# Performance work log

Hardware: AMD Instinct MI355X
Metric: run time of the kernel (lower is better)

Reference implementation:

```python
import jax, jax.numpy as jnp
import numpy as np

N = 50000      # nodes
E = 800000     # edges (before self-loops)
F_IN = 128     # raw node feature dim
D = 500        # GCN_in_dim = gcn_dim = h_mlp_dim
T = 200000     # number of triplets


def setup_inputs() -> dict:
    key = jax.random.key(0)
    ks = jax.random.split(key, 13)
    s = 0.05
    return {
        "feats": jax.random.normal(ks[0], (N, F_IN), jnp.float32),
        "W_aff": jax.random.normal(ks[1], (F_IN, D), jnp.float32) * s,
        "b_aff": jax.random.normal(ks[2], (D,), jnp.float32) * s,
        "W_gcn": jax.random.normal(ks[3], (D, D), jnp.float32) * s,
        "b_gcn": jax.random.normal(ks[4], (D,), jnp.float32) * s,
        "W_pred_in": jax.random.normal(ks[5], (2 * D, D), jnp.float32) * s,
        "b_pred_in": jax.random.normal(ks[6], (D,), jnp.float32) * s,
        "W_pred_out": jax.random.normal(ks[7], (D, 1), jnp.float32) * s,
        "b_pred_out": jax.random.normal(ks[8], (1,), jnp.float32) * s,
        "src": jax.random.randint(ks[9], (E,), 0, N),
        "dst": jax.random.randint(ks[10], (E,), 0, N),
        "triplets": jax.random.randint(ks[11], (T, 3), 0, N),
    }


def reference(feats, W_aff, b_aff, W_gcn, b_gcn, W_pred_in, b_pred_in,
              W_pred_out, b_pred_out, src, dst, triplets):
    n = feats.shape[0]
    # LinearAffine (use_pre_linearAffine=True)
    x = feats @ W_aff + b_aff                      # [N, D]

    # dgl.add_self_loop
    loop = jnp.arange(n)
    s_idx = jnp.concatenate([src, loop])
    d_idx = jnp.concatenate([dst, loop])

    # GraphConv, norm='both', no edge weights, activation=None
    ones = jnp.ones(s_idx.shape[0], jnp.float32)
    out_deg = jax.ops.segment_sum(ones, s_idx, num_segments=n)
    in_deg = jax.ops.segment_sum(ones, d_idx, num_segments=n)
    norm_src = jnp.where(out_deg > 0, jax.lax.rsqrt(out_deg), 0.0)  # [N]
    norm_dst = jnp.where(in_deg > 0, jax.lax.rsqrt(in_deg), 0.0)    # [N]

    xw = x @ W_gcn                                  # [N, D]
    msg = xw[s_idx] * norm_src[s_idx, None]         # [E+N, D] gather
    agg = jax.ops.segment_sum(msg, d_idx, num_segments=n)  # scatter-add
    embedding = agg * norm_dst[:, None] + b_gcn     # [N, D]

    # triplet gather + MLP_edge_predictor (layer_num=2: cat->Linear->Linear)
    s_feat = embedding[triplets[:, 0]]              # [T, D]
    o_feat = embedding[triplets[:, 2]]              # [T, D]
    t = jnp.concatenate([s_feat, o_feat], axis=-1) @ W_pred_in + b_pred_in
    weights = t @ W_pred_out + b_pred_out           # [T, 1]
    return (weights, embedding)
```

## Files before the change

kernel.cpp:

```cpp
#include <hip/hip_runtime.h>


typedef float f32x4 __attribute__((ext_vector_type(4)));
typedef short s16x8 __attribute__((ext_vector_type(8)));

__device__ __forceinline__ unsigned short f2bf(float f) {
    unsigned u = __float_as_uint(f);
    unsigned r = (u + 0x7FFFu + ((u >> 16) & 1u)) >> 16;
    return (unsigned short)r;
}

__device__ __forceinline__ void async_ld16(const void* g, void* lds) {
    __builtin_amdgcn_global_load_lds(
        (const __attribute__((address_space(1))) unsigned int*)g,
        (__attribute__((address_space(3))) unsigned int*)lds,
        16, 0, 0);
}

__global__ __launch_bounds__(256) void hist2_kernel(
    const int* __restrict__ src, const int* __restrict__ dst,
    int* __restrict__ bhist_src, int* __restrict__ bhist_dst, int E) {
    __shared__ int lhs[256], lhd[256];
    lhs[threadIdx.x] = 0;
    lhd[threadIdx.x] = 0;
    __syncthreads();
    const int stride = gridDim.x * blockDim.x;
    for (int e = blockIdx.x * blockDim.x + threadIdx.x; e < E; e += stride) {
        atomicAdd(&lhs[src[e] >> 8], 1);
        atomicAdd(&lhd[dst[e] >> 8], 1);
    }
    __syncthreads();
    int cs = lhs[threadIdx.x], cd = lhd[threadIdx.x];
    if (cs > 0) atomicAdd(&bhist_src[threadIdx.x], cs);
    if (cd > 0) atomicAdd(&bhist_dst[threadIdx.x], cd);
}

__global__ void bscan2_kernel(const int* __restrict__ bhist_src, const int* __restrict__ bhist_dst,
                              int* __restrict__ sbbase, int* __restrict__ sbcursor,
                              int* __restrict__ dbbase, int* __restrict__ dbcursor,
                              int nbuk, int E) {
    __shared__ int sv[256];
    const int tid = threadIdx.x;

    int c = (tid < nbuk) ? bhist_src[tid] : 0;
    sv[tid] = c;
    __syncthreads();
    for (int st = 1; st < 256; st <<= 1) {
        int t = (tid >= st) ? sv[tid - st] : 0;
        __syncthreads();
        sv[tid] += t;
        __syncthreads();
    }
    if (tid < nbuk) { int ex = sv[tid] - c; sbbase[tid] = ex; sbcursor[tid] = ex; }
    if (tid == 0) sbbase[nbuk] = E;
    __syncthreads();

    c = (tid < nbuk) ? bhist_dst[tid] : 0;
    sv[tid] = c;
    __syncthreads();
    for (int st = 1; st < 256; st <<= 1) {
        int t = (tid >= st) ? sv[tid - st] : 0;
        __syncthreads();
        sv[tid] += t;
        __syncthreads();
    }
    if (tid < nbuk) { int ex = sv[tid] - c; dbbase[tid] = ex; dbcursor[tid] = ex; }
    if (tid == 0) dbbase[nbuk] = E;
}

#define PCH 4096
__global__ __launch_bounds__(256) void fused_partition_kernel(
    const int* __restrict__ src, const int* __restrict__ dst,
    int* __restrict__ dcursor, unsigned long long* __restrict__ pairs,
    int* __restrict__ scursor, int* __restrict__ ssorted,
    int E, int nbuk) {
    __shared__ int lhist[256];
    __shared__ int lbase[256];
    __shared__ int gbase[256];
    __shared__ int scanv[256];
    __shared__ unsigned long long lpair[PCH];
    __shared__ unsigned char lbid[PCH];

    const int tid = threadIdx.x;
    const int c0 = blockIdx.x * PCH;
    int cnt = E - c0; if (cnt > PCH) cnt = PCH;

    int dv[16], sv[16], rk[16];

    lhist[tid] = 0;
    __syncthreads();
#pragma unroll
    for (int q = 0; q < 16; ++q) {
        int e = c0 + q * 256 + tid;
        if (e < E) {
            int d = dst[e];
            dv[q] = d;
            sv[q] = src[e];
            rk[q] = atomicAdd(&lhist[d >> 8], 1);
        } else {
            dv[q] = -1;
            sv[q] = -1;
        }
    }
    __syncthreads();

    int c = lhist[tid];
    scanv[tid] = c;
    __syncthreads();
    for (int st = 1; st < 256; st <<= 1) {
        int t = (tid >= st) ? scanv[tid - st] : 0;
        __syncthreads();
        scanv[tid] += t;
        __syncthreads();
    }
    lbase[tid] = scanv[tid] - c;
    if (tid < nbuk && c > 0) gbase[tid] = atomicAdd(&dcursor[tid], c);
    __syncthreads();

#pragma unroll
    for (int q = 0; q < 16; ++q) {
        if (dv[q] >= 0) {
            int b = dv[q] >> 8;
            int slot = lbase[b] + rk[q];
            lpair[slot] = ((unsigned long long)(unsigned)dv[q] << 32) | (unsigned)sv[q];
            lbid[slot] = (unsigned char)b;
        }
    }
    __syncthreads();

    for (int i = tid; i < cnt; i += 256) {
        int b = lbid[i];
        pairs[(long)gbase[b] + (i - lbase[b])] = lpair[i];
    }
    __syncthreads();

    int* lval = (int*)lpair;
    lhist[tid] = 0;
    __syncthreads();
#pragma unroll
    for (int q = 0; q < 16; ++q) {
        if (sv[q] >= 0) rk[q] = atomicAdd(&lhist[sv[q] >> 8], 1);
    }
    __syncthreads();

    c = lhist[tid];
    scanv[tid] = c;
    __syncthreads();
    for (int st = 1; st < 256; st <<= 1) {
        int t = (tid >= st) ? scanv[tid - st] : 0;
        __syncthreads();
        scanv[tid] += t;
        __syncthreads();
    }
    lbase[tid] = scanv[tid] - c;
    if (tid < nbuk && c > 0) gbase[tid] = atomicAdd(&scursor[tid], c);
    __syncthreads();

#pragma unroll
    for (int q = 0; q < 16; ++q) {
        if (sv[q] >= 0) {
            int b = sv[q] >> 8;
            int slot = lbase[b] + rk[q];
            lval[slot] = sv[q];
            lbid[slot] = (unsigned char)b;
        }
    }
    __syncthreads();

    for (int i = tid; i < cnt; i += 256) {
        int b = lbid[i];
        ssorted[(long)gbase[b] + (i - lbase[b])] = lval[i];
    }
}

__global__ __launch_bounds__(256) void bucket_finalize_kernel(
    const unsigned long long* __restrict__ pairs, const int* __restrict__ dbbase,
    const int* __restrict__ ssorted, const int* __restrict__ sbbase,
    int* __restrict__ row_ptr, float* __restrict__ ndv,
    int* __restrict__ csr_src, float* __restrict__ ns, int N) {
    __shared__ int hist[256];
    __shared__ int scanv[256];
    __shared__ int lcur[256];
    const int tid = threadIdx.x;
    const int b = blockIdx.x;
    const int node = b * 256 + tid;

    const int e0 = dbbase[b], e1 = dbbase[b + 1];
    hist[tid] = 0;
    __syncthreads();
    for (int e = e0 + tid; e < e1; e += 256) {
        int d = (int)(pairs[e] >> 32);
        atomicAdd(&hist[d & 255], 1);
    }
    __syncthreads();

    int c = hist[tid];
    scanv[tid] = c;
    __syncthreads();
    for (int st = 1; st < 256; st <<= 1) {
        int t = (tid >= st) ? scanv[tid - st] : 0;
        __syncthreads();
        scanv[tid] += t;
        __syncthreads();
    }
    int excl = scanv[tid] - c;
    if (node < N) {
        row_ptr[node] = e0 + excl;
        ndv[node] = rsqrtf((float)(c + 1));
    }
    if (node == N) row_ptr[N] = e0 + excl;
    lcur[tid] = excl;
    __syncthreads();

    for (int e = e0 + tid; e < e1; e += 256) {
        unsigned long long pr = pairs[e];
        int d = (int)(pr >> 32);
        int r = atomicAdd(&lcur[d & 255], 1);
        csr_src[e0 + r] = (int)(pr & 0xFFFFFFFFu);
    }

    __syncthreads();
    hist[tid] = 0;
    __syncthreads();
    const int s0 = sbbase[b], s1 = sbbase[b + 1];
    for (int e = s0 + tid; e < s1; e += 256) atomicAdd(&hist[ssorted[e] & 255], 1);
    __syncthreads();
    if (node < N) ns[node] = rsqrtf((float)(hist[tid] + 1));
}

__global__ __launch_bounds__(256) void bcomb_part_kernel(
    const float* __restrict__ b_aff, const float* __restrict__ W_gcn,
    float* __restrict__ part, int D, int PD) {
    int n = blockIdx.x * blockDim.x + threadIdx.x;
    int c = blockIdx.y;
    if (n >= PD) return;
    float s = 0.f;
    if (n < D) {
        int k0 = c * 8;
        int k1 = k0 + 8; if (k1 > D) k1 = D;
        for (int k = k0; k < k1; ++k) s = fmaf(b_aff[k], W_gcn[(long)k * D + n], s);
    }
    part[(long)c * PD + n] = s;
}

__global__ void vcomb_kernel(const float* __restrict__ Win, const float* __restrict__ wout,
                             float* __restrict__ v, int D, int K2) {
    int k = blockIdx.x * (blockDim.x >> 6) + (threadIdx.x >> 6);
    int lane = threadIdx.x & 63;
    if (k >= K2) return;
    float s = 0.f;
    for (int c = lane; c < D; c += 64) s = fmaf(Win[(long)k * D + c], wout[c], s);
#pragma unroll
    for (int m = 32; m > 0; m >>= 1) s += __shfl_down(s, m);
    if (lane == 0) v[k] = s;
}

__global__ void bias_dot_kernel(const float* __restrict__ b_in, const float* __restrict__ w_out,
                                const float* __restrict__ b_out, float* __restrict__ bias_dot, int D) {
    __shared__ float sm[256];
    float s = 0.f;
    for (int c = threadIdx.x; c < D; c += 256) s = fmaf(b_in[c], w_out[c], s);
    sm[threadIdx.x] = s;
    __syncthreads();
    for (int st = 128; st > 0; st >>= 1) {
        if (threadIdx.x < st) sm[threadIdx.x] += sm[threadIdx.x + st];
        __syncthreads();
    }
    if (threadIdx.x == 0) bias_dot[0] = sm[0] + b_out[0];
}

__global__ void pad_kernel(const float* __restrict__ part, const float* __restrict__ b_gcn,
                           const float* __restrict__ v, float* __restrict__ bcp,
                           float* __restrict__ bgp, float* __restrict__ v1p,
                           float* __restrict__ v2p, int D, int PD, int NC) {
    int i = blockIdx.x * blockDim.x + threadIdx.x;
    if (i < PD) {
        float s = 0.f;
        for (int c = 0; c < NC; ++c) s += part[(long)c * PD + i];
        bcp[i] = s;
        bgp[i] = (i < D) ? b_gcn[i] : 0.f;
        v1p[i] = (i < D) ? v[i] : 0.f;
        v2p[i] = (i < D) ? v[D + i] : 0.f;
    }
}

__global__ __launch_bounds__(256) void sgemm_kernel(const float* __restrict__ A, int lda,
                                                    const float* __restrict__ B, int ldb,
                                                    float* __restrict__ C, int ldc,
                                                    int M, int N, int K) {
    __shared__ __align__(16) float As[16][68];
    __shared__ __align__(16) float Bs[16][68];
    const int tid = threadIdx.x;
    const int tx = tid & 15, ty = tid >> 4;
    const int row0 = blockIdx.x * 64;
    const int col0 = blockIdx.y * 64;

    const int a_row = tid >> 2;
    const int a_k   = (tid & 3) * 4;
    const int b_k   = tid >> 4;
    const int b_c   = (tid & 15) * 4;

    float acc[4][4] = {};

    for (int k0 = 0; k0 < K; k0 += 16) {
        float4 av = make_float4(0.f, 0.f, 0.f, 0.f);
        {
            int gr = row0 + a_row;
            int gk = k0 + a_k;
            if (gr < M) {
                if (gk + 3 < K) {
                    av = *reinterpret_cast<const float4*>(&A[(long)gr * lda + gk]);
                } else {
                    float t0 = (gk + 0 < K) ? A[(long)gr * lda + gk + 0] : 0.f;
                    float t1 = (gk + 1 < K) ? A[(long)gr * lda + gk + 1] : 0.f;
                    float t2 = (gk + 2 < K) ? A[(long)gr * lda + gk + 2] : 0.f;
                    float t3 = (gk + 3 < K) ? A[(long)gr * lda + gk + 3] : 0.f;
                    av = make_float4(t0, t1, t2, t3);
                }
            }
        }
        float4 bv = make_float4(0.f, 0.f, 0.f, 0.f);
        {
            int gk = k0 + b_k;
            int gc = col0 + b_c;
            if (gk < K) {
                if (gc + 3 < N) {
                    bv = *reinterpret_cast<const float4*>(&B[(long)gk * ldb + gc]);
                } else {
                    float t0 = (gc + 0 < N) ? B[(long)gk * ldb + gc + 0] : 0.f;
                    float t1 = (gc + 1 < N) ? B[(long)gk * ldb + gc + 1] : 0.f;
                    float t2 = (gc + 2 < N) ? B[(long)gk * ldb + gc + 2] : 0.f;
                    float t3 = (gc + 3 < N) ? B[(long)gk * ldb + gc + 3] : 0.f;
                    bv = make_float4(t0, t1, t2, t3);
                }
            }
        }
        __syncthreads();
        As[a_k + 0][a_row] = av.x;
        As[a_k + 1][a_row] = av.y;
        As[a_k + 2][a_row] = av.z;
        As[a_k + 3][a_row] = av.w;
        *reinterpret_cast<float4*>(&Bs[b_k][b_c]) = bv;
        __syncthreads();

#pragma unroll
        for (int k = 0; k < 16; ++k) {
            const float4 a = *reinterpret_cast<const float4*>(&As[k][ty * 4]);
            const float4 b = *reinterpret_cast<const float4*>(&Bs[k][tx * 4]);
            const float avv[4] = {a.x, a.y, a.z, a.w};
            const float bvv[4] = {b.x, b.y, b.z, b.w};
#pragma unroll
            for (int i = 0; i < 4; ++i)
#pragma unroll
                for (int j = 0; j < 4; ++j)
                    acc[i][j] = fmaf(avv[i], bvv[j], acc[i][j]);
        }
    }

#pragma unroll
    for (int i = 0; i < 4; ++i) {
        int r = row0 + ty * 4 + i;
        if (r >= M) continue;
#pragma unroll
        for (int j = 0; j < 4; ++j) {
            int c = col0 + tx * 4 + j;
            if (c < N) C[(long)r * ldc + c] = acc[i][j];
        }
    }
}

__global__ void conv_feats_kernel(const float* __restrict__ feats, const float* __restrict__ ns,
                                  unsigned short* __restrict__ fs16, int N) {
    int idx = blockIdx.x * blockDim.x + threadIdx.x;
    if (idx >= N * 16) return;
    int node = idx >> 4;
    int c = (idx & 15) * 8;
    float s = ns[node];
    const float* p = feats + (long)node * 128 + c;
    float4 a = *reinterpret_cast<const float4*>(p);
    float4 b = *reinterpret_cast<const float4*>(p + 4);
    uint4 o;
    o.x = (unsigned)f2bf(a.x * s) | ((unsigned)f2bf(a.y * s) << 16);
    o.y = (unsigned)f2bf(a.z * s) | ((unsigned)f2bf(a.w * s) << 16);
    o.z = (unsigned)f2bf(b.x * s) | ((unsigned)f2bf(b.y * s) << 16);
    o.w = (unsigned)f2bf(b.z * s) | ((unsigned)f2bf(b.w * s) << 16);
    *reinterpret_cast<uint4*>(fs16 + (long)node * 128 + c) = o;
}

__global__ void conv_Bt_kernel(const float* __restrict__ Wc, unsigned short* __restrict__ Bt,
                               int D, int PD) {
    int idx = blockIdx.x * blockDim.x + threadIdx.x;
    if (idx >= PD * 16) return;
    int n = idx >> 4;
    int k8 = (idx & 15) * 8;
    uint4 o = make_uint4(0, 0, 0, 0);
    if (n < D) {
        unsigned short t[8];
#pragma unroll
        for (int q = 0; q < 8; ++q) t[q] = f2bf(Wc[(long)(k8 + q) * D + n]);
        o.x = (unsigned)t[0] | ((unsigned)t[1] << 16);
        o.y = (unsigned)t[2] | ((unsigned)t[3] << 16);
        o.z = (unsigned)t[4] | ((unsigned)t[5] << 16);
        o.w = (unsigned)t[6] | ((unsigned)t[7] << 16);
    }
    *reinterpret_cast<uint4*>(Bt + (long)n * 128 + k8) = o;
}

__global__ __launch_bounds__(256) void gather_feats_kernel(
    const unsigned short* __restrict__ fs16, const int* __restrict__ csr_src,
    const int* __restrict__ row_ptr, const float* __restrict__ ns,
    unsigned short* __restrict__ g16, float* __restrict__ h, int N) {
    int d = blockIdx.x * 4 + (threadIdx.x >> 6);
    int lane = threadIdx.x & 63;
    if (d >= N) return;
    const int g = lane >> 4;
    const int fl = lane & 15;

    float a[8] = {0.f, 0.f, 0.f, 0.f, 0.f, 0.f, 0.f, 0.f};
    float hacc = 0.f;

    const int beg = row_ptr[d], end = row_ptr[d + 1];
    for (int j0 = beg; j0 < end; j0 += 64) {
        int cnt = end - j0;
        if (cnt > 64) cnt = 64;
        int s = (lane < cnt) ? csr_src[j0 + lane] : 0;
        if (lane < cnt) hacc += ns[s];
        for (int k = 0; k < cnt; k += 8) {
            int k0 = k + g, k1 = k + 4 + g;
            int i0 = __shfl(s, k0 & 63);
            int i1 = __shfl(s, k1 & 63);
            uint4 v0 = make_uint4(0u, 0u, 0u, 0u), v1 = make_uint4(0u, 0u, 0u, 0u);
            if (k0 < cnt) v0 = *reinterpret_cast<const uint4*>(fs16 + (long)i0 * 128 + fl * 8);
            if (k1 < cnt) v1 = *reinterpret_cast<const uint4*>(fs16 + (long)i1 * 128 + fl * 8);
            a[0] += __uint_as_float(v0.x << 16); a[1] += __uint_as_float(v0.x & 0xFFFF0000u);
            a[2] += __uint_as_float(v0.y << 16); a[3] += __uint_as_float(v0.y & 0xFFFF0000u);
            a[4] += __uint_as_float(v0.z << 16); a[5] += __uint_as_float(v0.z & 0xFFFF0000u);
            a[6] += __uint_as_float(v0.w << 16); a[7] += __uint_as_float(v0.w & 0xFFFF0000u);
            a[0] += __uint_as_float(v1.x << 16); a[1] += __uint_as_float(v1.x & 0xFFFF0000u);
            a[2] += __uint_as_float(v1.y << 16); a[3] += __uint_as_float(v1.y & 0xFFFF0000u);
            a[4] += __uint_as_float(v1.z << 16); a[5] += __uint_as_float(v1.z & 0xFFFF0000u);
            a[6] += __uint_as_float(v1.w << 16); a[7] += __uint_as_float(v1.w & 0xFFFF0000u);
        }
    }

#pragma unroll
    for (int r = 0; r < 8; ++r) {
        a[r] += __shfl_xor(a[r], 16);
        a[r] += __shfl_xor(a[r], 32);
    }
    {
        uint4 sv4 = *reinterpret_cast<const uint4*>(fs16 + (long)d * 128 + fl * 8);
        a[0] += __uint_as_float(sv4.x << 16); a[1] += __uint_as_float(sv4.x & 0xFFFF0000u);
        a[2] += __uint_as_float(sv4.y << 16); a[3] += __uint_as_float(sv4.y & 0xFFFF0000u);
        a[4] += __uint_as_float(sv4.z << 16); a[5] += __uint_as_float(sv4.z & 0xFFFF0000u);
        a[6] += __uint_as_float(sv4.w << 16); a[7] += __uint_as_float(sv4.w & 0xFFFF0000u);
    }
#pragma unroll
    for (int m = 32; m > 0; m >>= 1) hacc += __shfl_xor(hacc, m);
    if (lane == 0) h[d] = hacc + ns[d];
    if (lane < 16) {
        uint4 o;
        o.x = (unsigned)f2bf(a[0]) | ((unsigned)f2bf(a[1]) << 16);
        o.y = (unsigned)f2bf(a[2]) | ((unsigned)f2bf(a[3]) << 16);
        o.z = (unsigned)f2bf(a[4]) | ((unsigned)f2bf(a[5]) << 16);
        o.w = (unsigned)f2bf(a[6]) | ((unsigned)f2bf(a[7]) << 16);
        *reinterpret_cast<uint4*>(g16 + (long)d * 128 + fl * 8) = o;
    }
}

__global__ __launch_bounds__(256) void gcn_gemm_kernel(
    const unsigned short* __restrict__ g16, const unsigned short* __restrict__ Bt,
    const float* __restrict__ h, const float* __restrict__ nd,
    const float* __restrict__ bcp, const float* __restrict__ bgp,
    const float* __restrict__ v1p, const float* __restrict__ v2p,
    float* __restrict__ emb, float* __restrict__ u1, float* __restrict__ u2,
    int M, int D) {

    __shared__ __align__(16) unsigned short As[128 * 32];
    __shared__ __align__(16) unsigned short Bs[128 * 32];

    const int tid  = threadIdx.x;
    const int w    = tid >> 6;
    const int lane = tid & 63;
    const int row0 = blockIdx.x * 128;
    const int col0 = blockIdx.y * 128;

    const int r0   = 2 * w * 16 + (lane >> 2);
    const int r1   = (2 * w + 1) * 16 + (lane >> 2);
    const int slot = lane & 3;
    const int c0   = slot ^ ((r0 >> 1) & 3);
    const int c1   = slot ^ ((r1 >> 1) & 3);

    const unsigned short* pA0 = g16 + (long)(row0 + r0) * 128 + c0 * 8;
    const unsigned short* pA1 = g16 + (long)(row0 + r1) * 128 + c1 * 8;
    const unsigned short* pB0 = Bt + (long)(col0 + r0) * 128 + c0 * 8;
    const unsigned short* pB1 = Bt + (long)(col0 + r1) * 128 + c1 * 8;

    unsigned short* dA0 = As + 2 * w * 512;
    unsigned short* dA1 = As + (2 * w + 1) * 512;
    unsigned short* dB0 = Bs + 2 * w * 512;
    unsigned short* dB1 = Bs + (2 * w + 1) * 512;

    const int wrow = (w & 1) * 64;
    const int wcol = (w >> 1) * 64;
    const int lm = lane & 15, q = lane >> 4;
    const s16x8* pa[4];
    const s16x8* pb[4];
#pragma unroll
    for (int i = 0; i < 4; ++i) {
        int r = wrow + i * 16 + lm;
        int cs = q ^ ((r >> 1) & 3);
        pa[i] = reinterpret_cast<const s16x8*>(As + r * 32 + cs * 8);
        int n = wcol + i * 16 + lm;
        int cs2 = q ^ ((n >> 1) & 3);
        pb[i] = reinterpret_cast<const s16x8*>(Bs + n * 32 + cs2 * 8);
    }

    f32x4 acc[4][4];
#pragma unroll
    for (int i = 0; i < 4; ++i)
#pragma unroll
        for (int j = 0; j < 4; ++j) acc[i][j] = (f32x4)0.f;

    for (int k0 = 0; k0 < 128; k0 += 32) {
        async_ld16(pA0 + k0, dA0);
        async_ld16(pA1 + k0, dA1);
        async_ld16(pB0 + k0, dB0);
        async_ld16(pB1 + k0, dB1);
        __syncthreads();

        s16x8 af[4], bf[4];
#pragma unroll
        for (int i = 0; i < 4; ++i) { af[i] = *pa[i]; bf[i] = *pb[i]; }
#pragma unroll
        for (int i = 0; i < 4; ++i)
#pragma unroll
            for (int j = 0; j < 4; ++j)
                acc[i][j] = __builtin_amdgcn_mfma_f32_16x16x32_bf16(af[i], bf[j], acc[i][j], 0, 0, 0);
        __syncthreads();
    }

    float bcv[4], bgv[4], w1[4], w2[4];
    int colv[4];
#pragma unroll
    for (int j = 0; j < 4; ++j) {
        int c = col0 + wcol + j * 16 + lm;
        colv[j] = c;
        bcv[j] = bcp[c];
        bgv[j] = bgp[c];
        w1[j] = v1p[c];
        w2[j] = v2p[c];
    }

#pragma unroll
    for (int i = 0; i < 4; ++i) {
        float p1[4], p2[4];
#pragma unroll
        for (int reg = 0; reg < 4; ++reg) {
            int row = row0 + wrow + i * 16 + q * 4 + reg;
            float hb = h[row];
            float sc = nd[row];
            float s1 = 0.f, s2 = 0.f;
#pragma unroll
            for (int j = 0; j < 4; ++j) {
                float o = fmaf(sc, acc[i][j][reg] + hb * bcv[j], bgv[j]);
                if (row < M && colv[j] < D) emb[(long)row * D + colv[j]] = o;
                s1 = fmaf(o, w1[j], s1);
                s2 = fmaf(o, w2[j], s2);
            }
            p1[reg] = s1;
            p2[reg] = s2;
        }
#pragma unroll
        for (int mask = 1; mask < 16; mask <<= 1)
#pragma unroll
            for (int reg = 0; reg < 4; ++reg) {
                p1[reg] += __shfl_xor(p1[reg], mask);
                p2[reg] += __shfl_xor(p2[reg], mask);
            }
        if (lm == 0) {
#pragma unroll
            for (int reg = 0; reg < 4; ++reg) {
                int row = row0 + wrow + i * 16 + q * 4 + reg;
                if (row < M) {
                    atomicAdd(&u1[row], p1[reg]);
                    atomicAdd(&u2[row], p2[reg]);
                }
            }
        }
    }
}

__global__ void weights_kernel(const int* __restrict__ trip, const float* __restrict__ u1,
                               const float* __restrict__ u2, const float* __restrict__ bdot,
                               float* __restrict__ w, int T) {
    int r = blockIdx.x * blockDim.x + threadIdx.x;
    if (r < T) {
        int s = trip[(long)r * 3 + 0];
        int o = trip[(long)r * 3 + 2];
        w[r] = u1[s] + u2[o] + bdot[0];
    }
}


extern "C" void kernel_launch(void* const* d_in, const int* in_sizes, int n_in,
                              void* d_out, int out_size, void* d_ws, size_t ws_size,
                              hipStream_t stream) {
    const float* feats      = (const float*)d_in[0];
    const float* W_aff      = (const float*)d_in[1];
    const float* b_aff      = (const float*)d_in[2];
    const float* W_gcn      = (const float*)d_in[3];
    const float* b_gcn      = (const float*)d_in[4];
    const float* W_pred_in  = (const float*)d_in[5];
    const float* b_pred_in  = (const float*)d_in[6];
    const float* W_pred_out = (const float*)d_in[7];
    const float* b_pred_out = (const float*)d_in[8];
    const int*   src        = (const int*)d_in[9];
    const int*   dst        = (const int*)d_in[10];
    const int*   trip       = (const int*)d_in[11];

    const int D = in_sizes[2];
    const int F = in_sizes[1] / D;
    const int N = in_sizes[0] / F;
    const int E = in_sizes[9];
    const int T = in_sizes[11] / 3;

    const int PD = 512;
    const int GX = (N + 127) / 128;
    const int Mpad = GX * 128;
    const int NC = (D + 7) / 8;
    const int NBUK = (N >> 8) + 1;

    float* weights = (float*)d_out;
    float* emb     = (float*)d_out + T;

    char* p = (char*)d_ws;
    unsigned short* fs16 = (unsigned short*)p;  p += (size_t)N * 128 * 2;
    unsigned short* g16  = (unsigned short*)p;  p += (size_t)Mpad * 128 * 2;
    unsigned long long* pairs = (unsigned long long*)p; p += (size_t)E * 8;
    int* ssorted = (int*)p;  p += (size_t)E * 4;
    unsigned short* Bt   = (unsigned short*)p;  p += (size_t)PD * 128 * 2;
    float* Wc   = (float*)p;  p += (size_t)F * D * 4;
    float* bparts = (float*)p;  p += (size_t)64 * PD * 4;
    float* bcp  = (float*)p;  p += PD * 4;
    float* bgp  = (float*)p;  p += PD * 4;
    float* v1p  = (float*)p;  p += PD * 4;
    float* v2p  = (float*)p;  p += PD * 4;
    float* v    = (float*)p;  p += 1024 * 4;
    float* bdot = (float*)p;  p += 16;
    float* ns   = (float*)p;  p += (size_t)N * 4;
    float* nd   = (float*)p;  p += (size_t)N * 4;
    float* h    = (float*)p;  p += (size_t)Mpad * 4;
    float* u1   = (float*)p;  p += (size_t)N * 4;
    float* u2   = (float*)p;  p += (size_t)N * 4;
    int* bhist_src = (int*)p;  p += 256 * 4;
    int* bhist_dst = (int*)p;  p += 256 * 4;
    int* sbbase   = (int*)p;  p += 260 * 4;
    int* sbcursor = (int*)p;  p += 256 * 4;
    int* dbbase   = (int*)p;  p += 260 * 4;
    int* dbcursor = (int*)p;  p += 256 * 4;
    int* row_ptr = (int*)p;  p += (size_t)(N + 1) * 4;
    int* csr_src = (int*)p;  p += (size_t)E * 4;

    hipMemsetAsync(bhist_src, 0, 512 * 4, stream);
    hipMemsetAsync(u1, 0, 2 * (size_t)N * sizeof(float), stream);
    hipMemsetAsync(g16 + (size_t)N * 128, 0, (size_t)(Mpad - N) * 128 * 2, stream);
    hipMemsetAsync(h + N, 0, (size_t)(Mpad - N) * 4, stream);

    hist2_kernel<<<256, 256, 0, stream>>>(src, dst, bhist_src, bhist_dst, E);
    bscan2_kernel<<<1, 256, 0, stream>>>(bhist_src, bhist_dst, sbbase, sbcursor,
                                         dbbase, dbcursor, NBUK, E);
    fused_partition_kernel<<<(E + PCH - 1) / PCH, 256, 0, stream>>>(
        src, dst, dbcursor, pairs, sbcursor, ssorted, E, NBUK);
    bucket_finalize_kernel<<<NBUK, 256, 0, stream>>>(pairs, dbbase, ssorted, sbbase,
                                                     row_ptr, nd, csr_src, ns, N);

    vcomb_kernel<<<(2 * D + 3) / 4, 256, 0, stream>>>(W_pred_in, W_pred_out, v, D, 2 * D);
    bias_dot_kernel<<<1, 256, 0, stream>>>(b_pred_in, W_pred_out, b_pred_out, bdot, D);

    {
        dim3 grid((F + 63) / 64, (D + 63) / 64);
        sgemm_kernel<<<grid, 256, 0, stream>>>(W_aff, D, W_gcn, D, Wc, D, F, D, D);
    }
    {
        dim3 grid((PD + 255) / 256, NC);
        bcomb_part_kernel<<<grid, 256, 0, stream>>>(b_aff, W_gcn, bparts, D, PD);
    }
    pad_kernel<<<(PD + 255) / 256, 256, 0, stream>>>(bparts, b_gcn, v, bcp, bgp, v1p, v2p, D, PD, NC);
    conv_Bt_kernel<<<(PD * 16 + 255) / 256, 256, 0, stream>>>(Wc, Bt, D, PD);

    conv_feats_kernel<<<(N * 16 + 255) / 256, 256, 0, stream>>>(feats, ns, fs16, N);

    gather_feats_kernel<<<(N + 3) / 4, 256, 0, stream>>>(fs16, csr_src, row_ptr, ns, g16, h, N);

    {
        dim3 grid(GX, PD / 128);
        gcn_gemm_kernel<<<grid, 256, 0, stream>>>(g16, Bt, h, nd, bcp, bgp, v1p, v2p,
                                                  emb, u1, u2, N, D);
    }

    weights_kernel<<<(T + 255) / 256, 256, 0, stream>>>(trip, u1, u2, bdot, weights, T);
}
```

Measured before the change: 354.9 us.

## Fuse small setup kernels, split-K the weight-combine GEMM, fold feature conversion

Four memsets become one init kernel. The three small prep kernels (bias combine, predictor vector, bias dot) are merged into one launch. The Bt conversion now runs together with the pad kernel, and the bf16 feature conversion is folded into bucket_finalize. The small W_aff@W_gcn SGEMM is split along K into 4 partial products that the conversion kernel sums, which raises parallelism for a tiny-grid GEMM. This cuts launch count and serial latency, at the cost of a larger workspace and extra partial-sum reads.

Result: faster. 315.2 us (-11.2%).

```diff
diff --git a/kernel.cpp b/kernel.cpp
--- a/kernel.cpp
+++ b/kernel.cpp
@@ -15,6 +15,18 @@
         (const __attribute__((address_space(1))) unsigned int*)g,
         (__attribute__((address_space(3))) unsigned int*)lds,
         16, 0, 0);
+}
+
+__global__ __launch_bounds__(256) void init_kernel(
+    float* __restrict__ u, int nU4, unsigned* __restrict__ gpad, int nG,
+    float* __restrict__ hpad, int nH, int* __restrict__ bh, int nB) {
+    const int stride = gridDim.x * blockDim.x;
+    const int i0 = blockIdx.x * blockDim.x + threadIdx.x;
+    for (int i = i0; i < nU4; i += stride)
+        *reinterpret_cast<float4*>(u + i * 4) = make_float4(0.f, 0.f, 0.f, 0.f);
+    for (int i = i0; i < nG; i += stride) gpad[i] = 0u;
+    for (int i = i0; i < nH; i += stride) hpad[i] = 0.f;
+    for (int i = i0; i < nB; i += stride) bh[i] = 0;
 }
 
 __global__ __launch_bounds__(256) void hist2_kernel(
@@ -176,11 +188,14 @@
 __global__ __launch_bounds__(256) void bucket_finalize_kernel(
     const unsigned long long* __restrict__ pairs, const int* __restrict__ dbbase,
     const int* __restrict__ ssorted, const int* __restrict__ sbbase,
+    const float* __restrict__ feats,
     int* __restrict__ row_ptr, float* __restrict__ ndv,
-    int* __restrict__ csr_src, float* __restrict__ ns, int N) {
+    int* __restrict__ csr_src, float* __restrict__ ns,
+    unsigned short* __restrict__ fs16, int N) {
     __shared__ int hist[256];
     __shared__ int scanv[256];
     __shared__ int lcur[256];
+    __shared__ float nsv[256];
     const int tid = threadIdx.x;
     const int b = blockIdx.x;
     const int node = b * 256 + tid;
@@ -225,68 +240,78 @@
     const int s0 = sbbase[b], s1 = sbbase[b + 1];
     for (int e = s0 + tid; e < s1; e += 256) atomicAdd(&hist[ssorted[e] & 255], 1);
     __syncthreads();
-    if (node < N) ns[node] = rsqrtf((float)(hist[tid] + 1));
-}
-
-__global__ __launch_bounds__(256) void bcomb_part_kernel(
+    float nsval = rsqrtf((float)(hist[tid] + 1));
+    nsv[tid] = nsval;
+    if (node < N) ns[node] = nsval;
+    __syncthreads();
+
+    for (int r0 = 0; r0 < 256; r0 += 16) {
+        int r = r0 + (tid >> 4);
+        int nn = b * 256 + r;
+        if (nn >= N) break;
+        int cq = (tid & 15) * 8;
+        float s = nsv[r];
+        const float* pf = feats + (long)nn * 128 + cq;
+        float4 a = *reinterpret_cast<const float4*>(pf);
+        float4 d2 = *reinterpret_cast<const float4*>(pf + 4);
+        uint4 o;
+        o.x = (unsigned)f2bf(a.x * s) | ((unsigned)f2bf(a.y * s) << 16);
+        o.y = (unsigned)f2bf(a.z * s) | ((unsigned)f2bf(a.w * s) << 16);
+        o.z = (unsigned)f2bf(d2.x * s) | ((unsigned)f2bf(d2.y * s) << 16);
+        o.w = (unsigned)f2bf(d2.z * s) | ((unsigned)f2bf(d2.w * s) << 16);
+        *reinterpret_cast<uint4*>(fs16 + (long)nn * 128 + cq) = o;
+    }
+}
+
+__global__ __launch_bounds__(256) void prep1_kernel(
     const float* __restrict__ b_aff, const float* __restrict__ W_gcn,
-    float* __restrict__ part, int D, int PD) {
-    int n = blockIdx.x * blockDim.x + threadIdx.x;
-    int c = blockIdx.y;
-    if (n >= PD) return;
-    float s = 0.f;
-    if (n < D) {
-        int k0 = c * 8;
-        int k1 = k0 + 8; if (k1 > D) k1 = D;
-        for (int k = k0; k < k1; ++k) s = fmaf(b_aff[k], W_gcn[(long)k * D + n], s);
-    }
-    part[(long)c * PD + n] = s;
-}
-
-__global__ void vcomb_kernel(const float* __restrict__ Win, const float* __restrict__ wout,
-                             float* __restrict__ v, int D, int K2) {
-    int k = blockIdx.x * (blockDim.x >> 6) + (threadIdx.x >> 6);
-    int lane = threadIdx.x & 63;
-    if (k >= K2) return;
-    float s = 0.f;
-    for (int c = lane; c < D; c += 64) s = fmaf(Win[(long)k * D + c], wout[c], s);
-#pragma unroll
-    for (int m = 32; m > 0; m >>= 1) s += __shfl_down(s, m);
-    if (lane == 0) v[k] = s;
-}
-
-__global__ void bias_dot_kernel(const float* __restrict__ b_in, const float* __restrict__ w_out,
-                                const float* __restrict__ b_out, float* __restrict__ bias_dot, int D) {
+    float* __restrict__ part,
+    const float* __restrict__ Win, const float* __restrict__ wout,
+    float* __restrict__ v,
+    const float* __restrict__ b_in, const float* __restrict__ b_out,
+    float* __restrict__ bdot,
+    int D, int PD, int NBbc, int NBv, int nbper) {
     __shared__ float sm[256];
-    float s = 0.f;
-    for (int c = threadIdx.x; c < D; c += 256) s = fmaf(b_in[c], w_out[c], s);
-    sm[threadIdx.x] = s;
-    __syncthreads();
-    for (int st = 128; st > 0; st >>= 1) {
-        if (threadIdx.x < st) sm[threadIdx.x] += sm[threadIdx.x + st];
-        __syncthreads();
-    }
-    if (threadIdx.x == 0) bias_dot[0] = sm[0] + b_out[0];
-}
-
-__global__ void pad_kernel(const float* __restrict__ part, const float* __restrict__ b_gcn,
-                           const float* __restrict__ v, float* __restrict__ bcp,
-                           float* __restrict__ bgp, float* __restrict__ v1p,
-                           float* __restrict__ v2p, int D, int PD, int NC) {
-    int i = blockIdx.x * blockDim.x + threadIdx.x;
-    if (i < PD) {
+    const int b = blockIdx.x;
+    const int tid = threadIdx.x;
+
+    if (b < NBbc) {
+        int nblk = b % nbper;
+        int cch = b / nbper;
+        int n = nblk * 256 + tid;
+        if (n >= PD) return;
         float s = 0.f;
-        for (int c = 0; c < NC; ++c) s += part[(long)c * PD + i];
-        bcp[i] = s;
-        bgp[i] = (i < D) ? b_gcn[i] : 0.f;
-        v1p[i] = (i < D) ? v[i] : 0.f;
-        v2p[i] = (i < D) ? v[D + i] : 0.f;
+        if (n < D) {
+            int k0 = cch * 8;
+            int k1 = k0 + 8; if (k1 > D) k1 = D;
+            for (int k = k0; k < k1; ++k) s = fmaf(b_aff[k], W_gcn[(long)k * D + n], s);
+        }
+        part[(long)cch * PD + n] = s;
+    } else if (b < NBbc + NBv) {
+        int k = (b - NBbc) * 4 + (tid >> 6);
+        int lane = tid & 63;
+        if (k >= 2 * D) return;
+        float s = 0.f;
+        for (int cc = lane; cc < D; cc += 64) s = fmaf(Win[(long)k * D + cc], wout[cc], s);
+#pragma unroll
+        for (int m = 32; m > 0; m >>= 1) s += __shfl_down(s, m);
+        if (lane == 0) v[k] = s;
+    } else {
+        float s = 0.f;
+        for (int cc = tid; cc < D; cc += 256) s = fmaf(b_in[cc], wout[cc], s);
+        sm[tid] = s;
+        __syncthreads();
+        for (int st = 128; st > 0; st >>= 1) {
+            if (tid < st) sm[tid] += sm[tid + st];
+            __syncthreads();
+        }
+        if (tid == 0) bdot[0] = sm[0] + b_out[0];
     }
 }
 
 __global__ __launch_bounds__(256) void sgemm_kernel(const float* __restrict__ A, int lda,
                                                     const float* __restrict__ B, int ldb,
-                                                    float* __restrict__ C, int ldc,
+                                                    float* __restrict__ Cp, int ldc,
                                                     int M, int N, int K) {
     __shared__ __align__(16) float As[16][68];
     __shared__ __align__(16) float Bs[16][68];
@@ -294,6 +319,9 @@
     const int tx = tid & 15, ty = tid >> 4;
     const int row0 = blockIdx.x * 64;
     const int col0 = blockIdx.y * 64;
+    const int kbeg = blockIdx.z * 128;
+    int kend = kbeg + 128; if (kend > K) kend = K;
+    float* C = Cp + (long)blockIdx.z * M * ldc;
 
     const int a_row = tid >> 2;
     const int a_k   = (tid & 3) * 4;
@@ -302,19 +330,19 @@
 
     float acc[4][4] = {};
 
-    for (int k0 = 0; k0 < K; k0 += 16) {
+    for (int k0 = kbeg; k0 < kend; k0 += 16) {
         float4 av = make_float4(0.f, 0.f, 0.f, 0.f);
         {
             int gr = row0 + a_row;
             int gk = k0 + a_k;
             if (gr < M) {
-                if (gk + 3 < K) {
+                if (gk + 3 < kend) {
                     av = *reinterpret_cast<const float4*>(&A[(long)gr * lda + gk]);
                 } else {
-                    float t0 = (gk + 0 < K) ? A[(long)gr * lda + gk + 0] : 0.f;
-                    float t1 = (gk + 1 < K) ? A[(long)gr * lda + gk + 1] : 0.f;
-                    float t2 = (gk + 2 < K) ? A[(long)gr * lda + gk + 2] : 0.f;
-                    float t3 = (gk + 3 < K) ? A[(long)gr * lda + gk + 3] : 0.f;
+                    float t0 = (gk + 0 < kend) ? A[(long)gr * lda + gk + 0] : 0.f;
+                    float t1 = (gk + 1 < kend) ? A[(long)gr * lda + gk + 1] : 0.f;
+                    float t2 = (gk + 2 < kend) ? A[(long)gr * lda + gk + 2] : 0.f;
+                    float t3 = (gk + 3 < kend) ? A[(long)gr * lda + gk + 3] : 0.f;
                     av = make_float4(t0, t1, t2, t3);
                 }
             }
@@ -323,7 +351,7 @@
         {
             int gk = k0 + b_k;
             int gc = col0 + b_c;
-            if (gk < K) {
+            if (gk < kend) {
                 if (gc + 3 < N) {
                     bv = *reinterpret_cast<const float4*>(&B[(long)gk * ldb + gc]);
                 } else {
@@ -369,41 +397,46 @@
     }
 }
 
-__global__ void conv_feats_kernel(const float* __restrict__ feats, const float* __restrict__ ns,
-                                  unsigned short* __restrict__ fs16, int N) {
-    int idx = blockIdx.x * blockDim.x + threadIdx.x;
-    if (idx >= N * 16) return;
-    int node = idx >> 4;
-    int c = (idx & 15) * 8;
-    float s = ns[node];
-    const float* p = feats + (long)node * 128 + c;
-    float4 a = *reinterpret_cast<const float4*>(p);
-    float4 b = *reinterpret_cast<const float4*>(p + 4);
-    uint4 o;
-    o.x = (unsigned)f2bf(a.x * s) | ((unsigned)f2bf(a.y * s) << 16);
-    o.y = (unsigned)f2bf(a.z * s) | ((unsigned)f2bf(a.w * s) << 16);
-    o.z = (unsigned)f2bf(b.x * s) | ((unsigned)f2bf(b.y * s) << 16);
-    o.w = (unsigned)f2bf(b.z * s) | ((unsigned)f2bf(b.w * s) << 16);
-    *reinterpret_cast<uint4*>(fs16 + (long)node * 128 + c) = o;
-}
-
-__global__ void conv_Bt_kernel(const float* __restrict__ Wc, unsigned short* __restrict__ Bt,
-                               int D, int PD) {
-    int idx = blockIdx.x * blockDim.x + threadIdx.x;
-    if (idx >= PD * 16) return;
-    int n = idx >> 4;
-    int k8 = (idx & 15) * 8;
-    uint4 o = make_uint4(0, 0, 0, 0);
-    if (n < D) {
-        unsigned short t[8];
-#pragma unroll
-        for (int q = 0; q < 8; ++q) t[q] = f2bf(Wc[(long)(k8 + q) * D + n]);
-        o.x = (unsigned)t[0] | ((unsigned)t[1] << 16);
-        o.y = (unsigned)t[2] | ((unsigned)t[3] << 16);
-        o.z = (unsigned)t[4] | ((unsigned)t[5] << 16);
-        o.w = (unsigned)t[6] | ((unsigned)t[7] << 16);
-    }
-    *reinterpret_cast<uint4*>(Bt + (long)n * 128 + k8) = o;
+__global__ __launch_bounds__(256) void convBt_pad_kernel(
+    const float* __restrict__ Wcp, unsigned short* __restrict__ Bt,
+    const float* __restrict__ part, const float* __restrict__ b_gcn,
+    const float* __restrict__ v, float* __restrict__ bcp,
+    float* __restrict__ bgp, float* __restrict__ v1p, float* __restrict__ v2p,
+    int D, int PD, int NC, int F, int nConvBlk) {
+    const int b = blockIdx.x;
+    const int tid = threadIdx.x;
+    if (b < nConvBlk) {
+        int idx = b * 256 + tid;
+        if (idx >= PD * 16) return;
+        int n = idx >> 4;
+        int k8 = (idx & 15) * 8;
+        uint4 o = make_uint4(0, 0, 0, 0);
+        if (n < D) {
+            unsigned short t[8];
+            const long FD = (long)F * D;
+#pragma unroll
+            for (int q = 0; q < 8; ++q) {
+                long off = (long)(k8 + q) * D + n;
+                float val = Wcp[off] + Wcp[FD + off] + Wcp[2 * FD + off] + Wcp[3 * FD + off];
+                t[q] = f2bf(val);
+            }
+            o.x = (unsigned)t[0] | ((unsigned)t[1] << 16);
+            o.y = (unsigned)t[2] | ((unsigned)t[3] << 16);
+            o.z = (unsigned)t[4] | ((unsigned)t[5] << 16);
+            o.w = (unsigned)t[6] | ((unsigned)t[7] << 16);
+        }
+        *reinterpret_cast<uint4*>(Bt + (long)n * 128 + k8) = o;
+    } else {
+        int i = (b - nConvBlk) * 256 + tid;
+        if (i < PD) {
+            float s = 0.f;
+            for (int c = 0; c < NC; ++c) s += part[(long)c * PD + i];
+            bcp[i] = s;
+            bgp[i] = (i < D) ? b_gcn[i] : 0.f;
+            v1p[i] = (i < D) ? v[i] : 0.f;
+            v2p[i] = (i < D) ? v[D + i] : 0.f;
+        }
+    }
 }
 
 __global__ __launch_bounds__(256) void gather_feats_kernel(
@@ -630,6 +663,7 @@
     const int Mpad = GX * 128;
     const int NC = (D + 7) / 8;
     const int NBUK = (N >> 8) + 1;
+    const int KS = 4;
 
     float* weights = (float*)d_out;
     float* emb     = (float*)d_out + T;
@@ -640,7 +674,7 @@
     unsigned long long* pairs = (unsigned long long*)p; p += (size_t)E * 8;
     int* ssorted = (int*)p;  p += (size_t)E * 4;
     unsigned short* Bt   = (unsigned short*)p;  p += (size_t)PD * 128 * 2;
-    float* Wc   = (float*)p;  p += (size_t)F * D * 4;
+    float* Wcp  = (float*)p;  p += (size_t)KS * F * D * 4;
     float* bparts = (float*)p;  p += (size_t)64 * PD * 4;
     float* bcp  = (float*)p;  p += PD * 4;
     float* bgp  = (float*)p;  p += PD * 4;
@@ -662,10 +696,11 @@
     int* row_ptr = (int*)p;  p += (size_t)(N + 1) * 4;
     int* csr_src = (int*)p;  p += (size_t)E * 4;
 
-    hipMemsetAsync(bhist_src, 0, 512 * 4, stream);
-    hipMemsetAsync(u1, 0, 2 * (size_t)N * sizeof(float), stream);
-    hipMemsetAsync(g16 + (size_t)N * 128, 0, (size_t)(Mpad - N) * 128 * 2, stream);
-    hipMemsetAsync(h + N, 0, (size_t)(Mpad - N) * 4, stream);
+    init_kernel<<<128, 256, 0, stream>>>(
+        u1, (2 * N) / 4,
+        (unsigned*)(g16 + (size_t)N * 128), (Mpad - N) * 128 / 2,
+        h + N, Mpad - N,
+        bhist_src, 512);
 
     hist2_kernel<<<256, 256, 0, stream>>>(src, dst, bhist_src, bhist_dst, E);
     bscan2_kernel<<<1, 256, 0, stream>>>(bhist_src, bhist_dst, sbbase, sbcursor,
@@ -673,23 +708,27 @@
     fused_partition_kernel<<<(E + PCH - 1) / PCH, 256, 0, stream>>>(
         src, dst, dbcursor, pairs, sbcursor, ssorted, E, NBUK);
     bucket_finalize_kernel<<<NBUK, 256, 0, stream>>>(pairs, dbbase, ssorted, sbbase,
-                                                     row_ptr, nd, csr_src, ns, N);
-
-    vcomb_kernel<<<(2 * D + 3) / 4, 256, 0, stream>>>(W_pred_in, W_pred_out, v, D, 2 * D);
-    bias_dot_kernel<<<1, 256, 0, stream>>>(b_pred_in, W_pred_out, b_pred_out, bdot, D);
+                                                     feats, row_ptr, nd, csr_src, ns,
+                                                     fs16, N);
 
     {
-        dim3 grid((F + 63) / 64, (D + 63) / 64);
-        sgemm_kernel<<<grid, 256, 0, stream>>>(W_aff, D, W_gcn, D, Wc, D, F, D, D);
+        const int nbper = (PD + 255) / 256;
+        const int NBbc = nbper * NC;
+        const int NBv = (2 * D + 3) / 4;
+        prep1_kernel<<<NBbc + NBv + 1, 256, 0, stream>>>(
+            b_aff, W_gcn, bparts, W_pred_in, W_pred_out, v,
+            b_pred_in, b_pred_out, bdot, D, PD, NBbc, NBv, nbper);
     }
     {
-        dim3 grid((PD + 255) / 256, NC);
-        bcomb_part_kernel<<<grid, 256, 0, stream>>>(b_aff, W_gcn, bparts, D, PD);
-    }
-    pad_kernel<<<(PD + 255) / 256, 256, 0, stream>>>(bparts, b_gcn, v, bcp, bgp, v1p, v2p, D, PD, NC);
-    conv_Bt_kernel<<<(PD * 16 + 255) / 256, 256, 0, stream>>>(Wc, Bt, D, PD);
-
-    conv_feats_kernel<<<(N * 16 + 255) / 256, 256, 0, stream>>>(feats, ns, fs16, N);
+        dim3 grid((F + 63) / 64, (D + 63) / 64, KS);
+        sgemm_kernel<<<grid, 256, 0, stream>>>(W_aff, D, W_gcn, D, Wcp, D, F, D, D);
+    }
+    {
+        const int nConvBlk = (PD * 16 + 255) / 256;
+        const int nPadBlk = (PD + 255) / 256;
+        convBt_pad_kernel<<<nConvBlk + nPadBlk, 256, 0, stream>>>(
+            Wcp, Bt, bparts, b_gcn, v, bcp, bgp, v1p, v2p, D, PD, NC, F, nConvBlk);
+    }
 
     gather_feats_kernel<<<(N + 3) / 4, 256, 0, stream>>>(fs16, csr_src, row_ptr, ns, g16, h, N);
 
```
